# Kernel tuning notes

Measured on AMD Instinct MI355X. Metric: run time of the kernel, lower is better.

## Reference

```python
import jax, jax.numpy as jnp
import numpy as np

B, C, N, K = 32, 1024, 2048, 64


def fps_indices(x, num):
    """Farthest-feature sampling. x: (B, N, C). Returns int32 indices (B, num).
    Deterministic start at index 0 (standard PointNet++ style loop)."""
    b, n, _ = x.shape

    def step(carry, _):
        dists, farthest = carry
        centroid = jnp.take_along_axis(x, farthest[:, None, None], axis=1)  # (B,1,C)
        d = jnp.sum((x - centroid) ** 2, axis=-1)  # (B,N)
        dists = jnp.minimum(dists, d)
        nxt = jnp.argmax(dists, axis=1).astype(jnp.int32)
        return (dists, nxt), farthest

    init = (jnp.full((b, n), 1e10, x.dtype), jnp.zeros((b,), jnp.int32))
    _, idx = jax.lax.scan(step, init, None, length=num)
    return idx.T  # (B, num)


def conv1x1(w, bias, x):
    # w: (out,in), x: (B,in,n) -> (B,out,n)
    return jnp.einsum('oi,bin->bon', w, x) + bias[:, None]


def setup_inputs() -> dict:
    key = jax.random.key(0)
    ks = jax.random.split(key, 16)
    s = 0.02
    return {
        'point_feat': jax.random.normal(ks[0], (B, C, N), jnp.float32),
        'global_feat': jax.random.normal(ks[1], (B, C), jnp.float32),
        'ps1_w': jax.random.normal(ks[2], (C, 128, K), jnp.float32) * s,
        'ps1_b': jnp.zeros((128,), jnp.float32),
        'm1c1_w': jax.random.normal(ks[3], (128, 2 * C + 128), jnp.float32) * s,
        'm1c1_b': jnp.zeros((128,), jnp.float32),
        'm1c2_w': jax.random.normal(ks[4], (128, 128), jnp.float32) * s,
        'm1c2_b': jnp.zeros((128,), jnp.float32),
        'm1sc_w': jax.random.normal(ks[5], (128, 2 * C + 128), jnp.float32) * s,
        'm1sc_b': jnp.zeros((128,), jnp.float32),
        'm2c1_w': jax.random.normal(ks[6], (64, 128), jnp.float32) * s,
        'm2c1_b': jnp.zeros((64,), jnp.float32),
        'm2c2_w': jax.random.normal(ks[7], (3, 64), jnp.float32) * s,
        'm2c2_b': jnp.zeros((3,), jnp.float32),
    }


def reference(point_feat, global_feat, ps1_w, ps1_b, m1c1_w, m1c1_b,
              m1c2_w, m1c2_b, m1sc_w, m1sc_b, m2c1_w, m2c1_b, m2c2_w, m2c2_b):
    # ffs: farthest-feature sample + gather
    xt = jnp.transpose(point_feat, (0, 2, 1))            # (B,N,C)
    idx = fps_indices(xt, K)                             # (B,K)
    feat_ffs = jnp.take_along_axis(xt, idx[:, :, None], axis=1)  # (B,K,C)
    feat_ffs = jnp.transpose(feat_ffs, (0, 2, 1))        # (B,C,K)

    # ConvTranspose1d on a length-1 input == outer product with kernel
    x1 = jnp.einsum('bi,iok->bok', global_feat, ps1_w) + ps1_b[:, None]  # (B,128,K)

    gf = jnp.broadcast_to(global_feat[:, :, None], (B, C, K))
    cat = jnp.concatenate([x1, feat_ffs, gf], axis=1)    # (B,2176,K)

    # MLP_Res
    shortcut = conv1x1(m1sc_w, m1sc_b, cat)
    h = conv1x1(m1c2_w, m1c2_b, jax.nn.relu(conv1x1(m1c1_w, m1c1_b, cat))) + shortcut

    # mlp_2
    pred = conv1x1(m2c2_w, m2c2_b, jax.nn.relu(conv1x1(m2c1_w, m2c1_b, h)))  # (B,3,K)
    return jnp.transpose(pred, (0, 2, 1))                # (B,K,3)
```

## Files before the change

kernel.cpp:

```cpp
#include <hip/hip_runtime.h>

#define BB_ 32
#define CC_ 1024
#define NN_ 2048
#define KK_ 64

typedef __bf16 bf16x8 __attribute__((ext_vector_type(8)));
typedef __bf16 bf16x2 __attribute__((ext_vector_type(2)));
typedef float f32x4 __attribute__((ext_vector_type(4)));
typedef unsigned int u32;

__device__ inline unsigned short f2bf_rn(float f) {
    unsigned u = __float_as_uint(f);
    unsigned r = (u + 0x7fffu + ((u >> 16) & 1u)) >> 16;
    return (unsigned short)r;
}

__device__ inline unsigned pack_bf16_rn(float f0, float f1) {
#if __has_builtin(__builtin_amdgcn_cvt_pk_bf16_f32)
    union { bf16x2 v; unsigned u; } x;
    x.v = __builtin_amdgcn_cvt_pk_bf16_f32(f0, f1);
    return x.u;
#else
    return (unsigned)f2bf_rn(f0) | ((unsigned)f2bf_rn(f1) << 16);
#endif
}

__device__ inline void split8(const float* f, uint4* H, uint4* L) {
    union { unsigned u[4]; uint4 v; } hq, lq;
#pragma unroll
    for (int j2 = 0; j2 < 4; j2++) {
        float a = f[2 * j2], c = f[2 * j2 + 1];
        unsigned hp = pack_bf16_rn(a, c);
        float h0f = __uint_as_float((hp & 0xffffu) << 16);
        float h1f = __uint_as_float(hp & 0xffff0000u);
        hq.u[j2] = hp;
        lq.u[j2] = pack_bf16_rn(a - h0f, c - h1f);
    }
    *H = hq.v; *L = lq.v;
}

__device__ inline void gload16(const void* g, void* l) {
    __builtin_amdgcn_global_load_lds(
        (const __attribute__((address_space(1))) u32*)g,
        (__attribute__((address_space(3))) u32*)l, 16, 0, 0);
}

__device__ void convert_body(const float* __restrict__ X,
                             unsigned char* __restrict__ Xc, int g0,
                             int cid, int t) {
    int chunk = cid & 7;
    int kt = (cid >> 3) & 31;
    int lb = cid >> 8;
    int n = chunk * 256 + t;
    int b = g0 + lb;
    const float* Xb = X + (size_t)b * CC_ * NN_;
    unsigned char* dst = Xc + (((size_t)lb * 32 + kt) * NN_ + n) * 128;
    int sw = n & 7;
#pragma unroll
    for (int q = 0; q < 4; q++) {
        float f[8];
#pragma unroll
        for (int j = 0; j < 8; j++)
            f[j] = Xb[(size_t)(kt * 32 + q * 8 + j) * NN_ + n];
        uint4 hq, lq;
        split8(f, &hq, &lq);
        int p = q ^ sw;
        *(uint4*)(dst + (p << 4)) = hq;
        *(uint4*)(dst + ((p ^ 4) << 4)) = lq;
    }
}

__global__ void convert_kernel(const float* __restrict__ X,
                               unsigned char* __restrict__ Xc, int g0) {
    convert_body(X, Xc, g0, blockIdx.x, threadIdx.x);
}

__device__ void fps_block(const float* Gb, int* idx, int b) {
    __shared__ float swv[2][4];
    __shared__ int swi[2][4];
    int t = threadIdx.x;
    float dist[8], nr[8];
#pragma unroll
    for (int r = 0; r < 8; r++) {
        nr[r] = Gb[(size_t)(t + 256 * r) * (NN_ + 1)];
        dist[r] = 1e10f;
    }
    if (t == 0) idx[b * KK_] = 0;
    int far = 0;
    for (int k = 1; k < KK_; k++) {
        float nf = Gb[(size_t)far * (NN_ + 1)];
        const float* grow = Gb + (size_t)far * NN_;
        float v = -1.f;
        int pi = 0;
#pragma unroll
        for (int r = 0; r < 8; r++) {
            float d = nr[r] + nf - 2.f * grow[t + 256 * r];
            dist[r] = fminf(dist[r], d);
            if (dist[r] > v) { v = dist[r]; pi = t + 256 * r; }
        }
#pragma unroll
        for (int off = 32; off; off >>= 1) {
            float ov = __shfl_down(v, off);
            int oi = __shfl_down(pi, off);
            if (ov > v || (ov == v && oi < pi)) { v = ov; pi = oi; }
        }
        int par = k & 1;
        if ((t & 63) == 0) { swv[par][t >> 6] = v; swi[par][t >> 6] = pi; }
        __syncthreads();
        float bv = swv[par][0];
        int bi = swi[par][0];
#pragma unroll
        for (int ww = 1; ww < 4; ww++) {
            float wv2 = swv[par][ww]; int wi2 = swi[par][ww];
            if (wv2 > bv || (wv2 == bv && wi2 < bi)) { bv = wv2; bi = wi2; }
        }
        far = bi;
        if (t == 0) idx[b * KK_ + k] = bi;
    }
}

__global__ __launch_bounds__(256, 2) void gram_fps_kernel(
    const unsigned char* __restrict__ Xc, float* __restrict__ G,
    const float* Gprev, int* __restrict__ idx, int nFps, int g0prev,
    const float* __restrict__ X, unsigned char* __restrict__ XcNext,
    int g0next, int nGram, int gs) {
    int bx = (int)blockIdx.x;
    if (bx < nFps) {
        fps_block(Gprev + (size_t)bx * NN_ * NN_, idx, g0prev + bx);
        return;
    }
    bx -= nFps;
    if (bx >= nGram) {
        convert_body(X, XcNext, g0next, bx - nGram, threadIdx.x);
        return;
    }
    int lb = bx % gs;
    int tt = bx / gs;
    int tn = (int)((sqrtf(8.f * tt + 1.f) - 1.f) * 0.5f);
    while ((tn + 1) * (tn + 2) / 2 <= tt) tn++;
    while (tn * (tn + 1) / 2 > tt) tn--;
    int tm = tt - tn * (tn + 1) / 2;
    bool diag = (tm == tn);
    int t = threadIdx.x;
    __shared__ __align__(16) unsigned char sMem[128 * 132 * 4];

    const unsigned char* XcB = Xc + (size_t)lb * 32 * NN_ * 128;
    int w = t >> 6, l = t & 63;
    int m0w = (w & 1) * 64, n0w = (w >> 1) * 64;
    int q = l >> 4, rr = l & 15;

    f32x4 zero = {0.f, 0.f, 0.f, 0.f};
    f32x4 acc[4][4];
#pragma unroll
    for (int mt = 0; mt < 4; mt++)
#pragma unroll
        for (int nt = 0; nt < 4; nt++) acc[mt][nt] = zero;

    auto stage = [&](int buf, int kt) {
        const unsigned char* Ab = XcB + ((size_t)kt * NN_ + (size_t)tm * 128) * 128;
        const unsigned char* Bb = XcB + ((size_t)kt * NN_ + (size_t)tn * 128) * 128;
        unsigned char* dA = sMem + buf * 32768;
        unsigned char* dB = dA + 16384;
#pragma unroll
        for (int r = 0; r < 4; r++) {
            gload16(Ab + r * 4096 + t * 16, dA + r * 4096 + t * 16);
            gload16(Bb + r * 4096 + t * 16, dB + r * 4096 + t * 16);
        }
    };

    stage(0, 0);
    for (int kt = 0; kt < 32; kt++) {
        int c = kt & 1;
        if (kt < 31) {
            stage(c ^ 1, kt + 1);
            asm volatile("s_waitcnt vmcnt(8)" ::: "memory");
        } else {
            asm volatile("s_waitcnt vmcnt(0)" ::: "memory");
        }
        __builtin_amdgcn_sched_barrier(0);
        __builtin_amdgcn_s_barrier();

        const unsigned char* cA = sMem + c * 32768;
        const unsigned char* cB = cA + 16384;
        bf16x8 ah[4], al[4], bh[4], bl[4];
#pragma unroll
        for (int mt = 0; mt < 4; mt++) {
            int ra = m0w + mt * 16 + rr;
            int pa = q ^ (ra & 7);
            ah[mt] = *(const bf16x8*)(cA + ra * 128 + (pa << 4));
            al[mt] = *(const bf16x8*)(cA + ra * 128 + ((pa ^ 4) << 4));
            int rb = n0w + mt * 16 + rr;
            int pb = q ^ (rb & 7);
            bh[mt] = *(const bf16x8*)(cB + rb * 128 + (pb << 4));
            bl[mt] = *(const bf16x8*)(cB + rb * 128 + ((pb ^ 4) << 4));
        }
#pragma unroll
        for (int mt = 0; mt < 4; mt++)
#pragma unroll
            for (int nt = 0; nt < 4; nt++) {
                acc[mt][nt] = __builtin_amdgcn_mfma_f32_16x16x32_bf16(ah[mt], bh[nt], acc[mt][nt], 0, 0, 0);
                acc[mt][nt] = __builtin_amdgcn_mfma_f32_16x16x32_bf16(ah[mt], bl[nt], acc[mt][nt], 0, 0, 0);
                acc[mt][nt] = __builtin_amdgcn_mfma_f32_16x16x32_bf16(al[mt], bh[nt], acc[mt][nt], 0, 0, 0);
            }
        __builtin_amdgcn_s_barrier();
    }

    float* Gb = G + (size_t)lb * NN_ * NN_;
    int i0 = tm * 128, j0 = tn * 128;
    int cc = l & 15;
    float* tb = (float*)sMem;
#pragma unroll
    for (int mt = 0; mt < 4; mt++)
#pragma unroll
        for (int nt = 0; nt < 4; nt++)
#pragma unroll
            for (int r = 0; r < 4; r++) {
                int gi = m0w + mt * 16 + q * 4 + r;
                int gj = n0w + nt * 16 + cc;
                float val = acc[mt][nt][r];
                Gb[(size_t)(i0 + gi) * NN_ + j0 + gj] = val;
                if (!diag) tb[gj * 132 + gi] = val;
            }
    if (!diag) {
        __syncthreads();
#pragma unroll
        for (int m = 0; m < 16; m++) {
            int f = t + 256 * m;
            int jj = f >> 5, sg = f & 31;
            float4 v4 = *(const float4*)(tb + jj * 132 + sg * 4);
            *(float4*)(&Gb[(size_t)(j0 + jj) * NN_ + i0 + sg * 4]) = v4;
        }
    }
}

__global__ void x1_fps_kernel(const float* __restrict__ gf, const float* __restrict__ w,
                              const float* __restrict__ bias, float* __restrict__ cat,
                              const float* Gprev, int* __restrict__ idx,
                              int g0prev, int nFps) {
    if ((int)blockIdx.x < nFps) {
        fps_block(Gprev + (size_t)blockIdx.x * NN_ * NN_, idx, g0prev + blockIdx.x);
        return;
    }
    int bid = blockIdx.x - nFps;
    int t = threadIdx.x;
    int okg = bid & 31, bg = bid >> 5;
    int ok = okg * 256 + t;
    int o = ok >> 6, k = ok & 63;
    float acc[8];
#pragma unroll
    for (int j = 0; j < 8; j++) acc[j] = 0.f;
    const float* g = gf + (size_t)(bg * 8) * CC_;
    for (int i = 0; i < CC_; i++) {
        float wv = w[(size_t)(i * 128 + o) * KK_ + k];
#pragma unroll
        for (int j = 0; j < 8; j++) acc[j] += g[j * CC_ + i] * wv;
    }
    float bv = bias[o];
#pragma unroll
    for (int j = 0; j < 8; j++)
        cat[((size_t)(bg * 8 + j) * 2176 + o) * KK_ + k] = acc[j] + bv;
}

__global__ void catfill_kernel(const float* __restrict__ X, const float* __restrict__ gf,
                               const int* __restrict__ idx, float* __restrict__ cat) {
    int b = blockIdx.y;
    int t = threadIdx.x;
    int ch = 128 + blockIdx.x * 4 + (t >> 6);
    int k = t & 63;
    float v;
    if (ch < 1152) {
        int c = ch - 128;
        int ik = idx[b * KK_ + k];
        v = X[((size_t)b * CC_ + c) * NN_ + ik];
    } else {
        v = gf[b * CC_ + (ch - 1152)];
    }
    cat[((size_t)b * 2176 + ch) * KK_ + k] = v;
}

__global__ void wconv_kernel(const float* __restrict__ w1, const float* __restrict__ wsc,
                             unsigned char* __restrict__ Wc) {
    int it = blockIdx.x;
    int m = threadIdx.x;
    const float* src = (m < 128 ? w1 + (size_t)m * 2176
                                : wsc + (size_t)(m - 128) * 2176) + it * 32;
    unsigned char* dst = Wc + ((size_t)it * 256 + m) * 128;
    int sw = m & 7;
#pragma unroll
    for (int q = 0; q < 4; q++) {
        float f[8];
        *(float4*)f       = *(const float4*)(src + q * 8);
        *(float4*)(f + 4) = *(const float4*)(src + q * 8 + 4);
        uint4 hq, lq;
        split8(f, &hq, &lq);
        int p = q ^ sw;
        *(uint4*)(dst + (p << 4)) = hq;
        *(uint4*)(dst + ((p ^ 4) << 4)) = lq;
    }
}

__global__ void cconv_kernel(const float* __restrict__ cat,
                             unsigned char* __restrict__ Cc) {
    int it = blockIdx.x, b = blockIdx.y;
    int t = threadIdx.x;
    int k = t & 63, q = t >> 6;
    const float* src = cat + (size_t)b * 2176 * KK_ + (size_t)(it * 32 + q * 8) * KK_ + k;
    float f[8];
#pragma unroll
    for (int j = 0; j < 8; j++) f[j] = src[j * KK_];
    uint4 hq, lq;
    split8(f, &hq, &lq);
    unsigned char* dst = Cc + (((size_t)b * 68 + it) * 64 + k) * 128;
    int p = q ^ (k & 7);
    *(uint4*)(dst + (p << 4)) = hq;
    *(uint4*)(dst + ((p ^ 4) << 4)) = lq;
}

__global__ __launch_bounds__(256, 2) void mlp1m_kernel(
    const unsigned char* __restrict__ Wc, const unsigned char* __restrict__ Cc,
    float* __restrict__ P) {
    int s = blockIdx.x & 3, b = blockIdx.x >> 2;
    int t = threadIdx.x;
    __shared__ __align__(16) unsigned char sMem[2 * 40960];
    int w = t >> 6, l = t & 63;
    int m0w = w * 64;
    int q = l >> 4, rr = l & 15;
    const unsigned char* WcS = Wc + (size_t)s * 17 * 32768;
    const unsigned char* CcS = Cc + ((size_t)b * 68 + s * 17) * 8192;

    f32x4 zero = {0.f, 0.f, 0.f, 0.f};
    f32x4 acc[4][4];
#pragma unroll
    for (int mt = 0; mt < 4; mt++)
#pragma unroll
        for (int nt = 0; nt < 4; nt++) acc[mt][nt] = zero;

    auto stage = [&](int buf, int kt) {
        const unsigned char* A = WcS + (size_t)kt * 32768;
        const unsigned char* Bc = CcS + (size_t)kt * 8192;
        unsigned char* dA = sMem + buf * 40960;
        unsigned char* dB = dA + 32768;
#pragma unroll
        for (int r = 0; r < 8; r++)
            gload16(A + r * 4096 + t * 16, dA + r * 4096 + t * 16);
#pragma unroll
        for (int r = 0; r < 2; r++)
            gload16(Bc + r * 4096 + t * 16, dB + r * 4096 + t * 16);
    };

    stage(0, 0);
    for (int kt = 0; kt < 17; kt++) {
        int c = kt & 1;
        if (kt < 16) {
            stage(c ^ 1, kt + 1);
            asm volatile("s_waitcnt vmcnt(10)" ::: "memory");
        } else {
            asm volatile("s_waitcnt vmcnt(0)" ::: "memory");
        }
        __builtin_amdgcn_sched_barrier(0);
        __builtin_amdgcn_s_barrier();

        const unsigned char* cA = sMem + c * 40960;
        const unsigned char* cB = cA + 32768;
        bf16x8 ah[4], al[4], bh[4], bl[4];
#pragma unroll
        for (int mt = 0; mt < 4; mt++) {
            int ra = m0w + mt * 16 + rr;
            int pa = q ^ (ra & 7);
            ah[mt] = *(const bf16x8*)(cA + ra * 128 + (pa << 4));
            al[mt] = *(const bf16x8*)(cA + ra * 128 + ((pa ^ 4) << 4));
            int rb = mt * 16 + rr;
            int pb = q ^ (rb & 7);
            bh[mt] = *(const bf16x8*)(cB + rb * 128 + (pb << 4));
            bl[mt] = *(const bf16x8*)(cB + rb * 128 + ((pb ^ 4) << 4));
        }
#pragma unroll
        for (int mt = 0; mt < 4; mt++)
#pragma unroll
            for (int nt = 0; nt < 4; nt++) {
                acc[mt][nt] = __builtin_amdgcn_mfma_f32_16x16x32_bf16(ah[mt], bh[nt], acc[mt][nt], 0, 0, 0);
                acc[mt][nt] = __builtin_amdgcn_mfma_f32_16x16x32_bf16(ah[mt], bl[nt], acc[mt][nt], 0, 0, 0);
                acc[mt][nt] = __builtin_amdgcn_mfma_f32_16x16x32_bf16(al[mt], bh[nt], acc[mt][nt], 0, 0, 0);
                acc[mt][nt] = __builtin_amdgcn_mfma_f32_16x16x32_bf16(al[mt], bl[nt], acc[mt][nt], 0, 0, 0);
            }
        __builtin_amdgcn_s_barrier();
    }

    float* Pb = P + (size_t)(s * 32 + b) * 256 * 64;
    int cc = l & 15;
#pragma unroll
    for (int mt = 0; mt < 4; mt++)
#pragma unroll
        for (int nt = 0; nt < 4; nt++)
#pragma unroll
            for (int r = 0; r < 4; r++) {
                int gi = m0w + mt * 16 + q * 4 + r;
                int gj = nt * 16 + cc;
                Pb[(size_t)gi * 64 + gj] = acc[mt][nt][r];
            }
}

__global__ void mred_kernel(const float* __restrict__ P, const float* __restrict__ b1,
                            const float* __restrict__ bsc, float* __restrict__ t1,
                            float* __restrict__ sc) {
    int pid = (int)blockIdx.x * 256 + threadIdx.x;
    int k = pid & 63, o = (pid >> 6) & 255, b = pid >> 14;
    const size_t SLAB = (size_t)32 * 256 * 64;
    size_t base = ((size_t)b * 256 + o) * 64 + k;
    float sum = P[base] + P[base + SLAB] + P[base + 2 * SLAB] + P[base + 3 * SLAB];
    if (o < 128) t1[((size_t)b * 128 + o) * KK_ + k] = fmaxf(sum + b1[o], 0.f);
    else         sc[((size_t)b * 128 + (o - 128)) * KK_ + k] = sum + bsc[o - 128];
}

__global__ void mlp1_kernel(const float* __restrict__ cat, const float* __restrict__ w1,
                            const float* __restrict__ b1, const float* __restrict__ wsc,
                            const float* __restrict__ bsc, float* __restrict__ t1,
                            float* __restrict__ sc) {
    __shared__ float red[2][16][64];
    int b = blockIdx.y, og = blockIdx.x;
    int t = threadIdx.x;
    int k = t & 63, sub = t >> 6;
    int o0 = og * 4;
    const float* cb = cat + (size_t)b * 2176 * KK_;
    float a1[4], a2[4];
#pragma unroll
    for (int j = 0; j < 4; j++) { a1[j] = 0.f; a2[j] = 0.f; }
    int iBeg = sub * 544;
    int off = (b & 7) * 68;
#pragma unroll 1
    for (int seg = 0; seg < 2; seg++) {
        int s0 = iBeg + (seg ? 0 : off);
        int s1 = seg ? iBeg + off : iBeg + 544;
        for (int i = s0; i < s1; i += 4) {
            float v0 = cb[(i + 0) * KK_ + k];
            float v1 = cb[(i + 1) * KK_ + k];
            float v2 = cb[(i + 2) * KK_ + k];
            float v3 = cb[(i + 3) * KK_ + k];
#pragma unroll
            for (int j = 0; j < 4; j++) {
                float4 wv = *(const float4*)(w1 + (size_t)(o0 + j) * 2176 + i);
                a1[j] += wv.x * v0 + wv.y * v1 + wv.z * v2 + wv.w * v3;
                float4 ws = *(const float4*)(wsc + (size_t)(o0 + j) * 2176 + i);
                a2[j] += ws.x * v0 + ws.y * v1 + ws.z * v2 + ws.w * v3;
            }
        }
    }
#pragma unroll
    for (int j = 0; j < 4; j++) {
        red[0][sub * 4 + j][k] = a1[j];
        red[1][sub * 4 + j][k] = a2[j];
    }
    __syncthreads();
#pragma unroll
    for (int p = t; p < 512; p += 256) {
        int m = p >> 8;
        int j = (p >> 6) & 3;
        int kk = p & 63;
        float s = red[m][j][kk] + red[m][4 + j][kk] + red[m][8 + j][kk] + red[m][12 + j][kk];
        int o = o0 + j;
        size_t oidx = ((size_t)b * 128 + o) * KK_ + kk;
        if (m == 0) t1[oidx] = fmaxf(s + b1[o], 0.f);
        else        sc[oidx] = s + bsc[o];
    }
}

__global__ void mlp2_kernel(const float* __restrict__ t1, const float* __restrict__ sc,
                            const float* __restrict__ w2, const float* __restrict__ b2,
                            const float* __restrict__ w3, const float* __restrict__ b3,
                            const float* __restrict__ w4, const float* __restrict__ b4,
                            float* __restrict__ out) {
    __shared__ float sT[128 * 64];
    __shared__ float sH[128 * 64];
    __shared__ float sR[64 * 64];
    int b = blockIdx.x, t = threadIdx.x;
    const float4* t1b4 = (const float4*)(t1 + (size_t)b * 8192);
    for (int j = t; j < 2048; j += 256) ((float4*)sT)[j] = t1b4[j];
    __syncthreads();
    int k = t & 63, og = t >> 6;
    const float* scb = sc + (size_t)b * 8192;

#pragma unroll
    for (int pass = 0; pass < 4; pass++) {
        int o0 = og * 32 + pass * 8;
        float acc[8];
#pragma unroll
        for (int j = 0; j < 8; j++) acc[j] = b2[o0 + j] + scb[(o0 + j) * 64 + k];
        for (int i4 = 0; i4 < 32; i4++) {
            float v0 = sT[(i4 * 4 + 0) * 64 + k];
            float v1 = sT[(i4 * 4 + 1) * 64 + k];
            float v2 = sT[(i4 * 4 + 2) * 64 + k];
            float v3 = sT[(i4 * 4 + 3) * 64 + k];
#pragma unroll
            for (int j = 0; j < 8; j++) {
                float4 wv = *(const float4*)(w2 + (size_t)(o0 + j) * 128 + i4 * 4);
                acc[j] += wv.x * v0 + wv.y * v1 + wv.z * v2 + wv.w * v3;
            }
        }
#pragma unroll
        for (int j = 0; j < 8; j++) sH[(o0 + j) * 64 + k] = acc[j];
    }
    __syncthreads();

#pragma unroll
    for (int pass = 0; pass < 2; pass++) {
        int o0 = og * 16 + pass * 8;
        float acc[8];
#pragma unroll
        for (int j = 0; j < 8; j++) acc[j] = b3[o0 + j];
        for (int i4 = 0; i4 < 32; i4++) {
            float v0 = sH[(i4 * 4 + 0) * 64 + k];
            float v1 = sH[(i4 * 4 + 1) * 64 + k];
            float v2 = sH[(i4 * 4 + 2) * 64 + k];
            float v3 = sH[(i4 * 4 + 3) * 64 + k];
#pragma unroll
            for (int j = 0; j < 8; j++) {
                float4 wv = *(const float4*)(w3 + (size_t)(o0 + j) * 128 + i4 * 4);
                acc[j] += wv.x * v0 + wv.y * v1 + wv.z * v2 + wv.w * v3;
            }
        }
#pragma unroll
        for (int j = 0; j < 8; j++) sR[(o0 + j) * 64 + k] = fmaxf(acc[j], 0.f);
    }
    __syncthreads();

    if (t < 192) {
        int o = t % 3;
        int kk = t / 3;
        float a0 = 0.f, a1 = 0.f, a2 = 0.f, a3 = 0.f;
        for (int i4 = 0; i4 < 16; i4++) {
            float4 wv = *(const float4*)(w4 + o * 64 + i4 * 4);
            a0 += wv.x * sR[(i4 * 4 + 0) * 64 + kk];
            a1 += wv.y * sR[(i4 * 4 + 1) * 64 + kk];
            a2 += wv.z * sR[(i4 * 4 + 2) * 64 + kk];
            a3 += wv.w * sR[(i4 * 4 + 3) * 64 + kk];
        }
        out[((size_t)b * KK_ + kk) * 3 + o] = b4[o] + ((a0 + a1) + (a2 + a3));
    }
}

extern "C" void kernel_launch(void* const* d_in, const int* in_sizes, int n_in,
                              void* d_out, int out_size, void* d_ws, size_t ws_size,
                              hipStream_t stream) {
    const float* X    = (const float*)d_in[0];
    const float* gf   = (const float*)d_in[1];
    const float* ps1w = (const float*)d_in[2];
    const float* ps1b = (const float*)d_in[3];
    const float* w1   = (const float*)d_in[4];
    const float* b1   = (const float*)d_in[5];
    const float* w2   = (const float*)d_in[6];
    const float* b2   = (const float*)d_in[7];
    const float* wsc  = (const float*)d_in[8];
    const float* bscp = (const float*)d_in[9];
    const float* w3   = (const float*)d_in[10];
    const float* b3   = (const float*)d_in[11];
    const float* w4   = (const float*)d_in[12];
    const float* b4   = (const float*)d_in[13];
    float* out = (float*)d_out;

    const size_t G_PER  = (size_t)NN_ * NN_ * 4;
    const size_t XC_PER = (size_t)32 * NN_ * 128;
    const size_t IDX_B  = (size_t)BB_ * KK_ * 4;
    const size_t CAT_B  = (size_t)BB_ * 2176 * KK_ * 4;
    const size_t T1_B   = (size_t)BB_ * 128 * KK_ * 4;
    size_t rest = IDX_B + CAT_B + 2 * T1_B;

    int gs = 1, merged = 0, pipe = 0;
    {
        const int tg[8]  = {8, 8, 4, 4, 2, 2, 1, 1};
        const int tmg[8] = {1, 1, 1, 1, 1, 1, 1, 0};
        const int tp[8]  = {1, 0, 1, 0, 1, 0, 0, 0};
        for (int i = 0; i < 8; i++) {
            size_t need = (size_t)(tmg[i] ? 2 : 1) * tg[i] * G_PER
                        + (size_t)(tp[i] ? 2 : 1) * tg[i] * XC_PER + rest;
            if (ws_size >= need) { gs = tg[i]; merged = tmg[i]; pipe = tp[i]; break; }
        }
    }

    char* ws = (char*)d_ws;
    float* Gbuf = (float*)ws;
    size_t gBufBytes = (size_t)(merged ? 2 : 1) * gs * G_PER;
    unsigned char* Xc0 = (unsigned char*)(ws + gBufBytes);
    unsigned char* Xc1 = Xc0 + (pipe ? (size_t)gs * XC_PER : 0);
    size_t xcBytes = (size_t)(pipe ? 2 : 1) * gs * XC_PER;
    char* p = (char*)Xc0 + xcBytes;
    int* idxws = (int*)p;    p += IDX_B;
    float* cat = (float*)p;  p += CAT_B;
    float* t1  = (float*)p;  p += T1_B;
    float* sc  = (float*)p;

    const size_t WC_B = (size_t)68 * 256 * 128;
    const size_t CC_B = (size_t)BB_ * 68 * 64 * 128;
    const size_t P_B  = (size_t)4 * BB_ * 256 * 64 * 4;
    char* scratch = nullptr;
    if (xcBytes >= WC_B + CC_B + P_B) scratch = (char*)Xc0;
    else if (gBufBytes >= WC_B + CC_B + P_B) scratch = (char*)Gbuf;

    int ng = BB_ / gs;
    size_t halfElems = (size_t)gs * NN_ * NN_;
    int nGram = gs * 136;
    int nConvAll = 256 * gs;

    if (pipe) convert_kernel<<<nConvAll, 256, 0, stream>>>(X, Xc0, 0);
    for (int g = 0; g < ng; g++) {
        int g0 = g * gs;
        unsigned char* Xcur  = (g & 1) ? Xc1 : Xc0;
        unsigned char* Xnext = (g & 1) ? Xc0 : Xc1;
        if (!pipe) {
            Xcur = Xc0;
            convert_kernel<<<nConvAll, 256, 0, stream>>>(X, Xc0, g0);
        }
        float* Gcur = Gbuf + (merged ? (size_t)(g & 1) * halfElems : 0);
        float* Gprev = Gbuf + (merged ? (size_t)((g & 1) ^ 1) * halfElems : 0);
        int nFps = (merged && g > 0) ? gs : 0;
        int nConv = (pipe && g < ng - 1) ? nConvAll : 0;
        gram_fps_kernel<<<nFps + nGram + nConv, 256, 0, stream>>>(
            Xcur, Gcur, Gprev, idxws, nFps, g0 - gs, X, Xnext, g0 + gs, nGram, gs);
        if (!merged) {
            gram_fps_kernel<<<gs, 256, 0, stream>>>(
                Xcur, Gcur, Gcur, idxws, gs, g0, X, Xnext, 0, 0, gs);
        }
    }
    int nFpsLast = merged ? gs : 0;
    float* Glast = Gbuf + (merged ? (size_t)((ng - 1) & 1) * halfElems : 0);
    x1_fps_kernel<<<nFpsLast + 128, 256, 0, stream>>>(
        gf, ps1w, ps1b, cat, Glast, idxws, BB_ - gs, nFpsLast);
    catfill_kernel<<<dim3(512, BB_), 256, 0, stream>>>(X, gf, idxws, cat);
    if (scratch) {
        unsigned char* Wc = (unsigned char*)scratch;
        unsigned char* Cc = Wc + WC_B;
        float* P = (float*)(Cc + CC_B);
        wconv_kernel<<<68, 256, 0, stream>>>(w1, wsc, Wc);
        cconv_kernel<<<dim3(68, BB_), 256, 0, stream>>>(cat, Cc);
        mlp1m_kernel<<<128, 256, 0, stream>>>(Wc, Cc, P);
        mred_kernel<<<2048, 256, 0, stream>>>(P, b1, bscp, t1, sc);
    } else {
        mlp1_kernel<<<dim3(32, BB_), 256, 0, stream>>>(cat, w1, b1, wsc, bscp, t1, sc);
    }
    mlp2_kernel<<<BB_, 256, 0, stream>>>(t1, sc, w2, b2, w3, b3, w4, b4, out);
}
```

Measured before the change: 1.177 ms.

## Interleave Gram-matrix prefetch loads with MFMA row groups and raise MFMA priority

The Gram kernel's main loop used to issue every next-tile global-to-LDS load up front and then read all fragments before a single MFMA block. It now splits the prefetch into four pairs, one issued between each 16-row MFMA group. LDS fragment reads are staggered with explicit lgkmcnt waits, and s_setprio is raised around the MFMA bursts. The aim is to overlap memory traffic with matrix math across waves. The cost is extra s_barriers per k-step and some fragile hand-tuned wait counts.

```diff
diff --git a/kernel.cpp b/kernel.cpp
--- a/kernel.cpp
+++ b/kernel.cpp
@@ -44,6 +44,28 @@
     __builtin_amdgcn_global_load_lds(
         (const __attribute__((address_space(1))) u32*)g,
         (__attribute__((address_space(3))) u32*)l, 16, 0, 0);
+}
+
+__device__ inline void rd_pair(const unsigned char* base, int row, int q,
+                               bf16x8* h, bf16x8* l) {
+    int p = q ^ (row & 7);
+    *h = *(const bf16x8*)(base + row * 128 + (p << 4));
+    *l = *(const bf16x8*)(base + row * 128 + ((p ^ 4) << 4));
+}
+
+__device__ inline void mfma_row(f32x4* accR, bf16x8 ah, bf16x8 al,
+                                const bf16x8* bh, const bf16x8* bl) {
+    __builtin_amdgcn_s_setprio(1);
+#pragma unroll
+    for (int nt = 0; nt < 4; nt++)
+        accR[nt] = __builtin_amdgcn_mfma_f32_16x16x32_bf16(ah, bh[nt], accR[nt], 0, 0, 0);
+#pragma unroll
+    for (int nt = 0; nt < 4; nt++)
+        accR[nt] = __builtin_amdgcn_mfma_f32_16x16x32_bf16(ah, bl[nt], accR[nt], 0, 0, 0);
+#pragma unroll
+    for (int nt = 0; nt < 4; nt++)
+        accR[nt] = __builtin_amdgcn_mfma_f32_16x16x32_bf16(al, bh[nt], accR[nt], 0, 0, 0);
+    __builtin_amdgcn_s_setprio(0);
 }
 
 __device__ void convert_body(const float* __restrict__ X,
@@ -157,52 +179,58 @@
 #pragma unroll
         for (int nt = 0; nt < 4; nt++) acc[mt][nt] = zero;
 
-    auto stage = [&](int buf, int kt) {
+    auto stage_pair = [&](int buf, int kt, int r) {
         const unsigned char* Ab = XcB + ((size_t)kt * NN_ + (size_t)tm * 128) * 128;
         const unsigned char* Bb = XcB + ((size_t)kt * NN_ + (size_t)tn * 128) * 128;
         unsigned char* dA = sMem + buf * 32768;
         unsigned char* dB = dA + 16384;
-#pragma unroll
-        for (int r = 0; r < 4; r++) {
-            gload16(Ab + r * 4096 + t * 16, dA + r * 4096 + t * 16);
-            gload16(Bb + r * 4096 + t * 16, dB + r * 4096 + t * 16);
-        }
+        gload16(Ab + r * 4096 + t * 16, dA + r * 4096 + t * 16);
+        gload16(Bb + r * 4096 + t * 16, dB + r * 4096 + t * 16);
     };
 
-    stage(0, 0);
+    stage_pair(0, 0, 0); stage_pair(0, 0, 1);
+    stage_pair(0, 0, 2); stage_pair(0, 0, 3);
+#pragma unroll 2
     for (int kt = 0; kt < 32; kt++) {
         int c = kt & 1;
-        if (kt < 31) {
-            stage(c ^ 1, kt + 1);
-            asm volatile("s_waitcnt vmcnt(8)" ::: "memory");
+        const unsigned char* cA = sMem + c * 32768;
+        const unsigned char* cB = cA + 16384;
+        bool pf = kt < 31;
+        if (pf) {
+            stage_pair(c ^ 1, kt + 1, 0);
+            asm volatile("s_waitcnt vmcnt(2)" ::: "memory");
         } else {
             asm volatile("s_waitcnt vmcnt(0)" ::: "memory");
         }
         __builtin_amdgcn_sched_barrier(0);
         __builtin_amdgcn_s_barrier();
-
-        const unsigned char* cA = sMem + c * 32768;
-        const unsigned char* cB = cA + 16384;
-        bf16x8 ah[4], al[4], bh[4], bl[4];
-#pragma unroll
-        for (int mt = 0; mt < 4; mt++) {
-            int ra = m0w + mt * 16 + rr;
-            int pa = q ^ (ra & 7);
-            ah[mt] = *(const bf16x8*)(cA + ra * 128 + (pa << 4));
-            al[mt] = *(const bf16x8*)(cA + ra * 128 + ((pa ^ 4) << 4));
-            int rb = n0w + mt * 16 + rr;
-            int pb = q ^ (rb & 7);
-            bh[mt] = *(const bf16x8*)(cB + rb * 128 + (pb << 4));
-            bl[mt] = *(const bf16x8*)(cB + rb * 128 + ((pb ^ 4) << 4));
-        }
-#pragma unroll
-        for (int mt = 0; mt < 4; mt++)
-#pragma unroll
-            for (int nt = 0; nt < 4; nt++) {
-                acc[mt][nt] = __builtin_amdgcn_mfma_f32_16x16x32_bf16(ah[mt], bh[nt], acc[mt][nt], 0, 0, 0);
-                acc[mt][nt] = __builtin_amdgcn_mfma_f32_16x16x32_bf16(ah[mt], bl[nt], acc[mt][nt], 0, 0, 0);
-                acc[mt][nt] = __builtin_amdgcn_mfma_f32_16x16x32_bf16(al[mt], bh[nt], acc[mt][nt], 0, 0, 0);
-            }
+        __builtin_amdgcn_sched_barrier(0);
+        bf16x8 bh[4], bl[4], ah0, al0, ah1, al1, ah2, al2, ah3, al3;
+#pragma unroll
+        for (int nt = 0; nt < 4; nt++)
+            rd_pair(cB, n0w + nt * 16 + rr, q, &bh[nt], &bl[nt]);
+        rd_pair(cA, m0w + 0 * 16 + rr, q, &ah0, &al0);
+        rd_pair(cA, m0w + 1 * 16 + rr, q, &ah1, &al1);
+        asm volatile("s_waitcnt lgkmcnt(2)" ::: "memory");
+        __builtin_amdgcn_sched_barrier(0);
+        mfma_row(acc[0], ah0, al0, bh, bl);
+        __builtin_amdgcn_s_barrier();
+        if (pf) stage_pair(c ^ 1, kt + 1, 1);
+        rd_pair(cA, m0w + 2 * 16 + rr, q, &ah2, &al2);
+        asm volatile("s_waitcnt lgkmcnt(2)" ::: "memory");
+        __builtin_amdgcn_sched_barrier(0);
+        mfma_row(acc[1], ah1, al1, bh, bl);
+        __builtin_amdgcn_s_barrier();
+        if (pf) stage_pair(c ^ 1, kt + 1, 2);
+        rd_pair(cA, m0w + 3 * 16 + rr, q, &ah3, &al3);
+        asm volatile("s_waitcnt lgkmcnt(2)" ::: "memory");
+        __builtin_amdgcn_sched_barrier(0);
+        mfma_row(acc[2], ah2, al2, bh, bl);
+        __builtin_amdgcn_s_barrier();
+        if (pf) stage_pair(c ^ 1, kt + 1, 3);
+        asm volatile("s_waitcnt lgkmcnt(0)" ::: "memory");
+        __builtin_amdgcn_sched_barrier(0);
+        mfma_row(acc[3], ah3, al3, bh, bl);
         __builtin_amdgcn_s_barrier();
     }
 
@@ -360,6 +388,7 @@
         }
         __builtin_amdgcn_sched_barrier(0);
         __builtin_amdgcn_s_barrier();
+        __builtin_amdgcn_sched_barrier(0);
 
         const unsigned char* cA = sMem + c * 40960;
         const unsigned char* cB = cA + 32768;
```

Result: slower. 1.285 ms (+9.2%).

## Fuse gather into bf16 split conversion and split mlp2 across K halves

Applied to the files above, without the earlier changes.

Adds a catfillc kernel that gathers the sampled features and global-feature broadcast and writes them straight into the swizzled hi/lo bf16 layout used by the matrix kernel. This skips writing and re-reading the fp32 cat tensor for those channels, and cconv now only converts the first 128 x1 channels. mlp2 is split into two blocks per batch, each covering 32 of the K columns, to use more CUs. A further sched_barrier is placed after the s_barrier in the matmul loop. The risk is that the gather in catfillc uses strided global reads.

```diff
diff --git a/kernel.cpp b/kernel.cpp
--- a/kernel.cpp
+++ b/kernel.cpp
@@ -279,6 +279,33 @@
     cat[((size_t)b * 2176 + ch) * KK_ + k] = v;
 }
 
+__global__ void catfillc_kernel(const float* __restrict__ X, const float* __restrict__ gf,
+                                const int* __restrict__ idx,
+                                unsigned char* __restrict__ Cc) {
+    int b = blockIdx.y, t = threadIdx.x;
+    int k = t & 63, cg = t >> 6;
+    int chunk = blockIdx.x * 4 + cg;
+    int ch0 = 128 + chunk * 8;
+    float f[8];
+    if (ch0 < 1152) {
+        int ik = idx[b * KK_ + k];
+        const float* Xb = X + ((size_t)b * CC_ + (ch0 - 128)) * NN_ + ik;
+#pragma unroll
+        for (int j = 0; j < 8; j++) f[j] = Xb[(size_t)j * NN_];
+    } else {
+        const float* g = gf + (size_t)b * CC_ + (ch0 - 1152);
+        *(float4*)f       = *(const float4*)g;
+        *(float4*)(f + 4) = *(const float4*)(g + 4);
+    }
+    uint4 hq, lq;
+    split8(f, &hq, &lq);
+    int it = ch0 >> 5, q = (ch0 >> 3) & 3;
+    unsigned char* dst = Cc + (((size_t)b * 68 + it) * 64 + k) * 128;
+    int p = q ^ (k & 7);
+    *(uint4*)(dst + (p << 4)) = hq;
+    *(uint4*)(dst + ((p ^ 4) << 4)) = lq;
+}
+
 __global__ void wconv_kernel(const float* __restrict__ w1, const float* __restrict__ wsc,
                              unsigned char* __restrict__ Wc) {
     int it = blockIdx.x;
@@ -360,6 +387,7 @@
         }
         __builtin_amdgcn_sched_barrier(0);
         __builtin_amdgcn_s_barrier();
+        __builtin_amdgcn_sched_barrier(0);
 
         const unsigned char* cA = sMem + c * 40960;
         const unsigned char* cB = cA + 32768;
@@ -470,27 +498,31 @@
                             const float* __restrict__ w3, const float* __restrict__ b3,
                             const float* __restrict__ w4, const float* __restrict__ b4,
                             float* __restrict__ out) {
-    __shared__ float sT[128 * 64];
-    __shared__ float sH[128 * 64];
-    __shared__ float sR[64 * 64];
-    int b = blockIdx.x, t = threadIdx.x;
-    const float4* t1b4 = (const float4*)(t1 + (size_t)b * 8192);
-    for (int j = t; j < 2048; j += 256) ((float4*)sT)[j] = t1b4[j];
+    __shared__ float sT[128 * 32];
+    __shared__ float sH[128 * 32];
+    __shared__ float sR[64 * 32];
+    int bx = blockIdx.x, t = threadIdx.x;
+    int b = bx >> 1, k0 = (bx & 1) * 32;
+    for (int j = t; j < 1024; j += 256) {
+        int row = j >> 3, c4 = (j & 7) * 4;
+        *(float4*)(sT + row * 32 + c4) =
+            *(const float4*)(t1 + (size_t)b * 8192 + row * 64 + k0 + c4);
+    }
     __syncthreads();
-    int k = t & 63, og = t >> 6;
+    int k = t & 31, og = t >> 5;
     const float* scb = sc + (size_t)b * 8192;
 
 #pragma unroll
-    for (int pass = 0; pass < 4; pass++) {
-        int o0 = og * 32 + pass * 8;
+    for (int pass = 0; pass < 2; pass++) {
+        int o0 = og * 16 + pass * 8;
         float acc[8];
 #pragma unroll
-        for (int j = 0; j < 8; j++) acc[j] = b2[o0 + j] + scb[(o0 + j) * 64 + k];
+        for (int j = 0; j < 8; j++) acc[j] = b2[o0 + j] + scb[(o0 + j) * 64 + k0 + k];
         for (int i4 = 0; i4 < 32; i4++) {
-            float v0 = sT[(i4 * 4 + 0) * 64 + k];
-            float v1 = sT[(i4 * 4 + 1) * 64 + k];
-            float v2 = sT[(i4 * 4 + 2) * 64 + k];
-            float v3 = sT[(i4 * 4 + 3) * 64 + k];
+            float v0 = sT[(i4 * 4 + 0) * 32 + k];
+            float v1 = sT[(i4 * 4 + 1) * 32 + k];
+            float v2 = sT[(i4 * 4 + 2) * 32 + k];
+            float v3 = sT[(i4 * 4 + 3) * 32 + k];
 #pragma unroll
             for (int j = 0; j < 8; j++) {
                 float4 wv = *(const float4*)(w2 + (size_t)(o0 + j) * 128 + i4 * 4);
@@ -498,21 +530,20 @@
             }
         }
 #pragma unroll
-        for (int j = 0; j < 8; j++) sH[(o0 + j) * 64 + k] = acc[j];
+        for (int j = 0; j < 8; j++) sH[(o0 + j) * 32 + k] = acc[j];
     }
     __syncthreads();
 
-#pragma unroll
-    for (int pass = 0; pass < 2; pass++) {
-        int o0 = og * 16 + pass * 8;
+    {
+        int o0 = og * 8;
         float acc[8];
 #pragma unroll
         for (int j = 0; j < 8; j++) acc[j] = b3[o0 + j];
         for (int i4 = 0; i4 < 32; i4++) {
-            float v0 = sH[(i4 * 4 + 0) * 64 + k];
-            float v1 = sH[(i4 * 4 + 1) * 64 + k];
-            float v2 = sH[(i4 * 4 + 2) * 64 + k];
-            float v3 = sH[(i4 * 4 + 3) * 64 + k];
+            float v0 = sH[(i4 * 4 + 0) * 32 + k];
+            float v1 = sH[(i4 * 4 + 1) * 32 + k];
+            float v2 = sH[(i4 * 4 + 2) * 32 + k];
+            float v3 = sH[(i4 * 4 + 3) * 32 + k];
 #pragma unroll
             for (int j = 0; j < 8; j++) {
                 float4 wv = *(const float4*)(w3 + (size_t)(o0 + j) * 128 + i4 * 4);
@@ -520,22 +551,22 @@
             }
         }
 #pragma unroll
-        for (int j = 0; j < 8; j++) sR[(o0 + j) * 64 + k] = fmaxf(acc[j], 0.f);
+        for (int j = 0; j < 8; j++) sR[(o0 + j) * 32 + k] = fmaxf(acc[j], 0.f);
     }
     __syncthreads();
 
-    if (t < 192) {
+    if (t < 96) {
         int o = t % 3;
         int kk = t / 3;
         float a0 = 0.f, a1 = 0.f, a2 = 0.f, a3 = 0.f;
         for (int i4 = 0; i4 < 16; i4++) {
             float4 wv = *(const float4*)(w4 + o * 64 + i4 * 4);
-            a0 += wv.x * sR[(i4 * 4 + 0) * 64 + kk];
-            a1 += wv.y * sR[(i4 * 4 + 1) * 64 + kk];
-            a2 += wv.z * sR[(i4 * 4 + 2) * 64 + kk];
-            a3 += wv.w * sR[(i4 * 4 + 3) * 64 + kk];
-        }
-        out[((size_t)b * KK_ + kk) * 3 + o] = b4[o] + ((a0 + a1) + (a2 + a3));
+            a0 += wv.x * sR[(i4 * 4 + 0) * 32 + kk];
+            a1 += wv.y * sR[(i4 * 4 + 1) * 32 + kk];
+            a2 += wv.z * sR[(i4 * 4 + 2) * 32 + kk];
+            a3 += wv.w * sR[(i4 * 4 + 3) * 32 + kk];
+        }
+        out[((size_t)b * KK_ + k0 + kk) * 3 + o] = b4[o] + ((a0 + a1) + (a2 + a3));
     }
 }
 
@@ -625,17 +656,18 @@
     float* Glast = Gbuf + (merged ? (size_t)((ng - 1) & 1) * halfElems : 0);
     x1_fps_kernel<<<nFpsLast + 128, 256, 0, stream>>>(
         gf, ps1w, ps1b, cat, Glast, idxws, BB_ - gs, nFpsLast);
-    catfill_kernel<<<dim3(512, BB_), 256, 0, stream>>>(X, gf, idxws, cat);
     if (scratch) {
         unsigned char* Wc = (unsigned char*)scratch;
         unsigned char* Cc = Wc + WC_B;
         float* P = (float*)(Cc + CC_B);
         wconv_kernel<<<68, 256, 0, stream>>>(w1, wsc, Wc);
-        cconv_kernel<<<dim3(68, BB_), 256, 0, stream>>>(cat, Cc);
+        cconv_kernel<<<dim3(4, BB_), 256, 0, stream>>>(cat, Cc);
+        catfillc_kernel<<<dim3(64, BB_), 256, 0, stream>>>(X, gf, idxws, Cc);
         mlp1m_kernel<<<128, 256, 0, stream>>>(Wc, Cc, P);
         mred_kernel<<<2048, 256, 0, stream>>>(P, b1, bscp, t1, sc);
     } else {
+        catfill_kernel<<<dim3(512, BB_), 256, 0, stream>>>(X, gf, idxws, cat);
         mlp1_kernel<<<dim3(32, BB_), 256, 0, stream>>>(cat, w1, b1, wsc, bscp, t1, sc);
     }
-    mlp2_kernel<<<BB_, 256, 0, stream>>>(t1, sc, w2, b2, w3, b3, w4, b4, out);
-}
+    mlp2_kernel<<<BB_ * 2, 256, 0, stream>>>(t1, sc, w2, b2, w3, b3, w4, b4, out);
+}
```

New measurement: 1.144 ms. -2.8%, faster.
